# Kernel tuning notes

Hardware: AMD Instinct MI355X
Metric: run time of the kernel (lower is better)

## Reference

```python
import math
import jax, jax.numpy as jnp
import numpy as np

B, M, N, D, H = 64, 5, 1000, 128, 8
KS = D // H
TANH_CLIP = 10.0

def setup_inputs() -> dict:
    key = jax.random.key(0)
    ks = jax.random.split(key, 12)
    mask = jax.random.randint(ks[8], (B, M, N), 0, 2).astype(bool)
    mask = mask.at[:, 0, 0].set(True)  # guarantee at least one feasible action per batch row
    return {
        'node_embeddings': jax.random.normal(ks[0], (B, N, D), jnp.float32),
        'fixed_context': jax.random.normal(ks[1], (B, 1, D), jnp.float32),
        'prev_node_embeddings': jax.random.normal(ks[2], (B, M, D), jnp.float32),
        'node_dynamic_features': jax.random.normal(ks[3], (B, M, N, 8), jnp.float32),
        'vehicle_dynamic_features': jax.random.normal(ks[4], (B, M, 3), jnp.float32),
        'glimpse_V_static': jax.random.normal(ks[5], (H, B, 1, N, KS), jnp.float32),
        'glimpse_K_static': jax.random.normal(ks[6], (H, B, 1, N, KS), jnp.float32),
        'logit_K_static': jax.random.normal(ks[7], (B, 1, N, D), jnp.float32),
        'feasibility_mask': mask,
        'W_pcv': jax.random.normal(ks[9], (D, D + 3), jnp.float32) * 0.05,
        'W_pns': jax.random.normal(ks[10], (3 * D, 8), jnp.float32) * 0.05,
        'po_weight': jax.random.normal(ks[11], (D, D), jnp.float32) * 0.05,
    }

def reference(node_embeddings, fixed_context, prev_node_embeddings,
              node_dynamic_features, vehicle_dynamic_features,
              glimpse_V_static, glimpse_K_static, logit_K_static,
              feasibility_mask, W_pcv, W_pns, po_weight):
    # current vehicle state projection: [B,M,D]
    cvs = jnp.concatenate([prev_node_embeddings, vehicle_dynamic_features], axis=-1)
    proj_cvs = cvs @ W_pcv.T
    # dynamic node embeddings: [B,M,N,3D] -> three [B,M,N,D] chunks
    nde = node_dynamic_features @ W_pns.T
    gVd, gKd, lKd = jnp.split(nde, 3, axis=-1)
    # make heads: [B,M,N,D] -> [H,B,M,N,KS]
    def mh(x):
        return x.reshape(B, M, N, H, KS).transpose(3, 0, 1, 2, 4)
    glimpse_V = glimpse_V_static + mh(gVd)  # [H,B,M,N,KS]
    glimpse_K = glimpse_K_static + mh(gKd)
    logit_K = logit_K_static + lKd          # [B,M,N,D]
    query = fixed_context + proj_cvs        # [B,M,D]
    Q = query.reshape(B, M, H, KS).transpose(2, 0, 1, 3)  # [H,B,M,KS]
    mask_log = jnp.log(feasibility_mask.astype(jnp.float32))  # [B,M,N]
    compat = jnp.einsum('hbmk,hbmnk->hbmn', Q, glimpse_K) / math.sqrt(KS)
    compat = compat + mask_log[None]
    # softmax over joint vehicle*node axis
    attn = jax.nn.softmax(compat.reshape(H, B, M * N), axis=-1).reshape(H, B, M, N)
    heads = jnp.einsum('hbmn,hbmnk->hbmk', attn, glimpse_V)  # [H,B,M,KS]
    concat = heads.transpose(1, 2, 0, 3).reshape(B, M, D)
    final_Q = concat @ po_weight.T          # [B,M,D]
    logits = jnp.einsum('bmd,bmnd->bmn', final_Q, logit_K) / math.sqrt(D)
    logits = jnp.tanh(logits) * TANH_CLIP + mask_log
    probs = jax.nn.softmax(logits.reshape(B, M * N), axis=-1)
    return probs
```

## Files before the change

### kernel.cpp

```cpp
#include <hip/hip_runtime.h>
#include <cstddef>

#define BB 64
#define MM 5
#define NN 1000
#define DD 128
#define HH 8
#define KSZ 16
#define NCH 8
#define CH2 125
#define NC3 16
#define CH3 63
#define INV_SQRT_D 0.08838834764831845f

__device__ __forceinline__ float tanh_fast(float x) {
  float e = __expf(2.f * x);
  return 1.f - 2.f / (e + 1.f);
}

__global__ __launch_bounds__(256) void k1_query(
    const float* __restrict__ fc, const float* __restrict__ pne,
    const float* __restrict__ vdf, const float* __restrict__ wpcv,
    const float* __restrict__ wpns, const int* __restrict__ mask,
    float* __restrict__ q_ws, float* __restrict__ qw_ws,
    unsigned int* __restrict__ pmask)
{
  const int t = threadIdx.x;
  if (blockIdx.x >= BB * 4) {
    const int b = blockIdx.x - BB * 4;
    const int* mb = mask + (size_t)(b * MM) * NN;
    for (int n = t; n < NN; n += 256) {
      unsigned int pm = 0;
#pragma unroll
      for (int m = 0; m < MM; ++m) pm |= (mb[m * NN + n] != 0 ? 1u : 0u) << m;
      pmask[b * NN + n] = pm;
    }
    return;
  }
  const int b = blockIdx.x >> 2;
  const int dq = blockIdx.x & 3;
  const int k = t & 15, gid = t >> 4;
  __shared__ float qsh[MM][32];

  float cvr[9];
  int curm = -1;
  for (int r = 0; r < 10; ++r) {
    const int m = r >> 1;
    if (m != curm) {
      curm = m;
      const float* pner = pne + (size_t)(b * MM + m) * DD;
#pragma unroll
      for (int jp = 0; jp < 8; ++jp) cvr[jp] = pner[k + 16 * jp];
      cvr[8] = (k < 3) ? vdf[(b * MM + m) * 3 + k] : 0.f;
    }
    const int dl = (r & 1) * 16 + gid;
    const int d = dq * 32 + dl;
    const float* wrow = wpcv + d * 131;
    float p = 0.f;
#pragma unroll
    for (int jp = 0; jp < 8; ++jp) p = fmaf(cvr[jp], wrow[k + 16 * jp], p);
    if (k < 3) p = fmaf(cvr[8], wrow[128 + k], p);
    p += __shfl_xor(p, 1); p += __shfl_xor(p, 2);
    p += __shfl_xor(p, 4); p += __shfl_xor(p, 8);
    if (k == 0) {
      const float q = 0.25f * (p + fc[b * DD + d]);
      qsh[m][dl] = q;
      q_ws[(size_t)(b * MM + m) * DD + d] = q;
    }
  }
  __syncthreads();
  if (t < 80) {
    const int hh = t / 40;
    const int r = t - hh * 40, m = r >> 3, f = r & 7;
    const int h = dq * 2 + hh;
    float acc = 0.f;
#pragma unroll
    for (int kk = 0; kk < KSZ; ++kk)
      acc = fmaf(qsh[m][hh * 16 + kk], wpns[(DD + h * KSZ + kk) * 8 + f], acc);
    qw_ws[(b * HH + h) * 40 + m * 8 + f] = acc;
  }
}

__global__ __launch_bounds__(256, 4) void k2_attn(
    const float* __restrict__ ndf, const float* __restrict__ gV,
    const float* __restrict__ gK, const unsigned int* __restrict__ pmask,
    const float* __restrict__ q_ws, const float* __restrict__ qw_ws,
    float* __restrict__ part)
{
  const int blk = blockIdx.x;
  const int xcd = blk & 7;
  const int rest = blk >> 3;
  const int c = rest & 7;
  const int h = (rest >> 3) & 7;
  const int b = (rest >> 6) * 8 + xcd;
  const int t = threadIdx.x;
  const int k = t & 3, gid = t >> 2;
  const int n0 = c * CH2;

  const float* kb = gK + ((size_t)(h * BB + b) * NN + n0) * KSZ + 4 * k;
  const float* vb = gV + ((size_t)(h * BB + b) * NN + n0) * KSZ + 4 * k;
  const float* nb = ndf + ((size_t)(b * MM) * NN + n0) * 8 + 2 * k;
  const unsigned int* pmb = pmask + b * NN + n0;

  const int n1 = gid;
  const bool v2 = (gid < CH2 - 64);
  const int n2 = v2 ? gid + 64 : 0;
  const unsigned int pm1 = pmb[n1];
  const unsigned int pm2 = v2 ? pmb[n2] : 0u;
  const float4 kv1 = *(const float4*)(kb + n1 * KSZ);
  const float4 kv2 = *(const float4*)(kb + n2 * KSZ);
  const float4 vv1 = *(const float4*)(vb + n1 * KSZ);
  const float4 vv2 = *(const float4*)(vb + n2 * KSZ);
  float2 nd1[MM], nd2[MM];
#pragma unroll
  for (int m = 0; m < MM; ++m) {
    nd1[m] = *(const float2*)(nb + ((size_t)m * NN + n1) * 8);
    nd2[m] = *(const float2*)(nb + ((size_t)m * NN + n2) * 8);
  }

  float4 qr[MM];
  float2 qwr[MM];
#pragma unroll
  for (int m = 0; m < MM; ++m) {
    qr[m] = *(const float4*)(q_ws + (size_t)(b * MM + m) * DD + h * KSZ + 4 * k);
    qwr[m] = *(const float2*)(qw_ws + (b * HH + h) * 40 + m * 8 + 2 * k);
  }

  float4 hacc[MM] = {};
  float2 afv[MM] = {};
  float lsum = 0.f;

#pragma unroll
  for (int m = 0; m < MM; ++m) {
    float p = kv1.x * qr[m].x + kv1.y * qr[m].y
            + kv1.z * qr[m].z + kv1.w * qr[m].w
            + nd1[m].x * qwr[m].x + nd1[m].y * qwr[m].y;
    p += __shfl_xor(p, 1); p += __shfl_xor(p, 2);
    const float e = ((pm1 >> m) & 1u) ? __expf(p) : 0.f;
    hacc[m].x = fmaf(e, vv1.x, hacc[m].x);
    hacc[m].y = fmaf(e, vv1.y, hacc[m].y);
    hacc[m].z = fmaf(e, vv1.z, hacc[m].z);
    hacc[m].w = fmaf(e, vv1.w, hacc[m].w);
    afv[m].x = fmaf(e, nd1[m].x, afv[m].x);
    afv[m].y = fmaf(e, nd1[m].y, afv[m].y);
    lsum += e;
  }
#pragma unroll
  for (int m = 0; m < MM; ++m) {
    float p = kv2.x * qr[m].x + kv2.y * qr[m].y
            + kv2.z * qr[m].z + kv2.w * qr[m].w
            + nd2[m].x * qwr[m].x + nd2[m].y * qwr[m].y;
    p += __shfl_xor(p, 1); p += __shfl_xor(p, 2);
    const float e = ((pm2 >> m) & 1u) ? __expf(p) : 0.f;
    hacc[m].x = fmaf(e, vv2.x, hacc[m].x);
    hacc[m].y = fmaf(e, vv2.y, hacc[m].y);
    hacc[m].z = fmaf(e, vv2.z, hacc[m].z);
    hacc[m].w = fmaf(e, vv2.w, hacc[m].w);
    afv[m].x = fmaf(e, nd2[m].x, afv[m].x);
    afv[m].y = fmaf(e, nd2[m].y, afv[m].y);
    lsum += e;
  }

#pragma unroll
  for (int m = 0; m < MM; ++m) {
#pragma unroll
    for (int off = 4; off <= 32; off <<= 1) {
      hacc[m].x += __shfl_xor(hacc[m].x, off);
      hacc[m].y += __shfl_xor(hacc[m].y, off);
      hacc[m].z += __shfl_xor(hacc[m].z, off);
      hacc[m].w += __shfl_xor(hacc[m].w, off);
      afv[m].x += __shfl_xor(afv[m].x, off);
      afv[m].y += __shfl_xor(afv[m].y, off);
    }
  }
#pragma unroll
  for (int off = 4; off <= 32; off <<= 1) lsum += __shfl_xor(lsum, off);

  __shared__ float redh[4][MM][KSZ];
  __shared__ float redaf[4][MM][8];
  __shared__ float reds[4];
  const int w = t >> 6;
  if ((t & 63) < 4) {
    const int kk = t & 3;
#pragma unroll
    for (int m = 0; m < MM; ++m) {
      redh[w][m][4 * kk + 0] = hacc[m].x;
      redh[w][m][4 * kk + 1] = hacc[m].y;
      redh[w][m][4 * kk + 2] = hacc[m].z;
      redh[w][m][4 * kk + 3] = hacc[m].w;
      redaf[w][m][2 * kk + 0] = afv[m].x;
      redaf[w][m][2 * kk + 1] = afv[m].y;
    }
  }
  if ((t & 63) == 0) reds[w] = lsum;
  __syncthreads();
  float* P = part + (size_t)((b * NCH + c) * HH + h) * 128;
  if (t < 80) {
    const int m = t >> 4, kk = t & 15;
    P[t] = redh[0][m][kk] + redh[1][m][kk] + redh[2][m][kk] + redh[3][m][kk];
  } else if (t < 120) {
    const int r = t - 80, m = r >> 3, f = r & 7;
    P[80 + r] = redaf[0][m][f] + redaf[1][m][f] + redaf[2][m][f] + redaf[3][m][f];
  } else if (t == 120) {
    P[120] = reds[0] + reds[1] + reds[2] + reds[3];
  }
}

__global__ __launch_bounds__(256) void k2b_combine(
    const float* __restrict__ part, const float* __restrict__ wpns,
    const float* __restrict__ po, float* __restrict__ fq_ws,
    float* __restrict__ fw_ws)
{
  const int b = blockIdx.x;
  const int t = threadIdx.x;
  __shared__ float pos[DD][129];
  __shared__ float rgs[HH];
  __shared__ float afs[HH][MM][8];
  __shared__ float cs[MM][DD];
  __shared__ float fqs[MM][DD];

  for (int i = t; i < DD * DD / 4; i += 256) {
    const float4 v = ((const float4*)po)[i];
    const int r = (i * 4) >> 7, cc = (i * 4) & 127;
    pos[r][cc] = v.x; pos[r][cc + 1] = v.y; pos[r][cc + 2] = v.z; pos[r][cc + 3] = v.w;
  }
  const float* pb = part + (size_t)b * NCH * HH * 128;
  if (t < HH) {
    float s = 0.f;
#pragma unroll
    for (int c = 0; c < NCH; ++c) s += pb[(c * HH + t) * 128 + 120];
    rgs[t] = 1.f / s;
  }
  for (int idx = t; idx < HH * MM * 8; idx += 256) {
    const int h = idx / 40, r = idx % 40;
    float a = 0.f;
#pragma unroll
    for (int c = 0; c < NCH; ++c) a += pb[(c * HH + h) * 128 + 80 + r];
    afs[h][r >> 3][r & 7] = a;
  }
  __syncthreads();
  for (int idx = t; idx < MM * DD; idx += 256) {
    const int m = idx >> 7, d = idx & 127, h = d >> 4;
    float a = 0.f;
#pragma unroll
    for (int c = 0; c < NCH; ++c) a += pb[(c * HH + h) * 128 + m * 16 + (d & 15)];
    float cf = 0.f;
#pragma unroll
    for (int f = 0; f < 8; ++f) cf = fmaf(wpns[d * 8 + f], afs[h][m][f], cf);
    cs[m][d] = (a + cf) * rgs[h];
  }
  __syncthreads();
  for (int idx = t; idx < MM * DD; idx += 256) {
    const int m = idx >> 7, d = idx & 127;
    float acc = 0.f;
#pragma unroll 8
    for (int j = 0; j < DD; ++j) acc = fmaf(cs[m][j], pos[d][j], acc);
    acc *= INV_SQRT_D;
    fqs[m][d] = acc;
    fq_ws[(size_t)b * (MM * DD) + idx] = acc;
  }
  __syncthreads();
  if (t < MM * 8) {
    const int m = t >> 3, f = t & 7;
    float acc = 0.f;
#pragma unroll 16
    for (int d = 0; d < DD; ++d) acc = fmaf(fqs[m][d], wpns[(2 * DD + d) * 8 + f], acc);
    fw_ws[b * 40 + t] = acc;
  }
}

__global__ __launch_bounds__(256, 4) void k3_logits(
    const float* __restrict__ ndf, const float* __restrict__ lK,
    const unsigned int* __restrict__ pmask, const float* __restrict__ fq_ws,
    const float* __restrict__ fw_ws, float* __restrict__ out,
    float* __restrict__ stats)
{
  const int b = blockIdx.x & 63;
  const int c = blockIdx.x >> 6;
  const int t = threadIdx.x;
  const int k = t & 15, gid = t >> 4;
  const int n0 = c * CH3;

  float4 fqr[MM][2];
  float fwr[MM];
#pragma unroll
  for (int m = 0; m < MM; ++m) {
    fqr[m][0] = *(const float4*)(fq_ws + (size_t)(b * MM + m) * DD + 8 * k);
    fqr[m][1] = *(const float4*)(fq_ws + (size_t)(b * MM + m) * DD + 8 * k + 4);
    fwr[m] = fw_ws[b * 40 + m * 8 + (k & 7)];
  }
  float lsum = 0.f;

#pragma unroll
  for (int half = 0; half < 2; ++half) {
    float4 l0[2], l1[2];
    float ndv[2][MM];
    unsigned int pm[2];
    int ng[2];
    bool vld[2];
#pragma unroll
    for (int j = 0; j < 2; ++j) {
      const int nl = gid + 16 * (half * 2 + j);
      const int n = n0 + nl;
      vld[j] = (nl < CH3) && (n < NN);
      const int nc = vld[j] ? n : n0;
      ng[j] = nc;
      pm[j] = vld[j] ? pmask[b * NN + nc] : 0u;
      const float* lkr = lK + ((size_t)b * NN + nc) * DD;
      l0[j] = *(const float4*)(lkr + 8 * k);
      l1[j] = *(const float4*)(lkr + 8 * k + 4);
#pragma unroll
      for (int m = 0; m < MM; ++m)
        ndv[j][m] = (k < 8) ? ndf[((size_t)(b * MM + m) * NN + nc) * 8 + k] : 0.f;
    }
#pragma unroll
    for (int j = 0; j < 2; ++j) {
#pragma unroll
      for (int m = 0; m < MM; ++m) {
        float p = l0[j].x * fqr[m][0].x + l0[j].y * fqr[m][0].y
                + l0[j].z * fqr[m][0].z + l0[j].w * fqr[m][0].w
                + l1[j].x * fqr[m][1].x + l1[j].y * fqr[m][1].y
                + l1[j].z * fqr[m][1].z + l1[j].w * fqr[m][1].w
                + ndv[j][m] * fwr[m];
        p += __shfl_xor(p, 1); p += __shfl_xor(p, 2);
        p += __shfl_xor(p, 4); p += __shfl_xor(p, 8);
        const float e = ((pm[j] >> m) & 1u) ? __expf(tanh_fast(p) * 10.f) : 0.f;
        if (vld[j]) {
          lsum += e;
          if (k == 0) out[(size_t)(b * MM + m) * NN + ng[j]] = e;
        }
      }
    }
  }
  lsum += __shfl_xor(lsum, 16);
  lsum += __shfl_xor(lsum, 32);
  __shared__ float wred[4];
  if ((t & 63) == 0) wred[t >> 6] = lsum;
  __syncthreads();
  if (t == 0)
    stats[b * NC3 + c] = wred[0] + wred[1] + wred[2] + wred[3];
}

__global__ __launch_bounds__(256) void k4_probs(
    const float* __restrict__ stats, float* __restrict__ out)
{
  const int bm = blockIdx.x;
  const int b = bm / MM;
  const int t = threadIdx.x;
  float s = 0.f;
#pragma unroll
  for (int c = 0; c < NC3; ++c) s += stats[b * NC3 + c];
  const float scale = 1.f / s;
  if (t < 250) {
    float4* p = (float4*)(out + (size_t)bm * NN);
    float4 v = p[t];
    v.x *= scale; v.y *= scale; v.z *= scale; v.w *= scale;
    p[t] = v;
  }
}

extern "C" void kernel_launch(void* const* d_in, const int* in_sizes, int n_in,
                              void* d_out, int out_size, void* d_ws, size_t ws_size,
                              hipStream_t stream) {
  const float* fc   = (const float*)d_in[1];
  const float* pne  = (const float*)d_in[2];
  const float* ndf  = (const float*)d_in[3];
  const float* vdf  = (const float*)d_in[4];
  const float* gV   = (const float*)d_in[5];
  const float* gK   = (const float*)d_in[6];
  const float* lK   = (const float*)d_in[7];
  const int*   mask = (const int*)d_in[8];
  const float* wpcv = (const float*)d_in[9];
  const float* wpns = (const float*)d_in[10];
  const float* po   = (const float*)d_in[11];

  float* q_ws  = (float*)d_ws;
  float* qw_ws = q_ws + BB * MM * DD;
  float* part  = qw_ws + BB * HH * 40;
  float* fq_ws = part + (size_t)BB * NCH * HH * 128;
  float* fw_ws = fq_ws + BB * MM * DD;
  float* stats = fw_ws + BB * 40;
  unsigned int* pmask = (unsigned int*)(stats + BB * NC3);
  float* out   = (float*)d_out;

  k1_query<<<BB * 4 + BB, 256, 0, stream>>>(fc, pne, vdf, wpcv, wpns, mask,
                                            q_ws, qw_ws, pmask);
  k2_attn<<<BB * HH * NCH, 256, 0, stream>>>(ndf, gV, gK, pmask, q_ws, qw_ws, part);
  k2b_combine<<<BB, 256, 0, stream>>>(part, wpns, po, fq_ws, fw_ws);
  k3_logits<<<BB * NC3, 256, 0, stream>>>(ndf, lK, pmask, fq_ws, fw_ws, out, stats);
  k4_probs<<<BB * MM, 256, 0, stream>>>(stats, out);
}
```

Measured before the change: 69.03 us.

## Restructure attention kernel so each block covers all heads and stages node features in LDS

Measured after the change: 83.58 us. +21.1%, slower.

```diff
diff --git a/kernel.cpp b/kernel.cpp
--- a/kernel.cpp
+++ b/kernel.cpp
@@ -7,8 +7,8 @@
 #define DD 128
 #define HH 8
 #define KSZ 16
-#define NCH 8
-#define CH2 125
+#define NCH 16
+#define CH2 63
 #define NC3 16
 #define CH3 63
 #define INV_SQRT_D 0.08838834764831845f
@@ -81,128 +81,135 @@
   }
 }
 
-__global__ __launch_bounds__(256, 4) void k2_attn(
+__global__ __launch_bounds__(256, 3) void k2_attn(
     const float* __restrict__ ndf, const float* __restrict__ gV,
     const float* __restrict__ gK, const unsigned int* __restrict__ pmask,
     const float* __restrict__ q_ws, const float* __restrict__ qw_ws,
     float* __restrict__ part)
 {
-  const int blk = blockIdx.x;
-  const int xcd = blk & 7;
-  const int rest = blk >> 3;
-  const int c = rest & 7;
-  const int h = (rest >> 3) & 7;
-  const int b = (rest >> 6) * 8 + xcd;
-  const int t = threadIdx.x;
-  const int k = t & 3, gid = t >> 2;
+  const int bid = blockIdx.x;
+  const int xcd = bid & 7;
+  const int rr = bid >> 3;
+  const int c = rr & 15;
+  const int b = (rr >> 4) * 8 + xcd;
+  const int t = threadIdx.x;
+  const int w = t >> 6;
+  const int lane = t & 63;
+  const int k = t & 3;
+  const int gid = (t >> 2) & 15;
   const int n0 = c * CH2;
-
-  const float* kb = gK + ((size_t)(h * BB + b) * NN + n0) * KSZ + 4 * k;
-  const float* vb = gV + ((size_t)(h * BB + b) * NN + n0) * KSZ + 4 * k;
-  const float* nb = ndf + ((size_t)(b * MM) * NN + n0) * 8 + 2 * k;
-  const unsigned int* pmb = pmask + b * NN + n0;
-
-  const int n1 = gid;
-  const bool v2 = (gid < CH2 - 64);
-  const int n2 = v2 ? gid + 64 : 0;
-  const unsigned int pm1 = pmb[n1];
-  const unsigned int pm2 = v2 ? pmb[n2] : 0u;
-  const float4 kv1 = *(const float4*)(kb + n1 * KSZ);
-  const float4 kv2 = *(const float4*)(kb + n2 * KSZ);
-  const float4 vv1 = *(const float4*)(vb + n1 * KSZ);
-  const float4 vv2 = *(const float4*)(vb + n2 * KSZ);
-  float2 nd1[MM], nd2[MM];
+  const int nvalid = (NN - n0 < CH2) ? (NN - n0) : CH2;
+
+  __shared__ float nlds[CH2][MM][8];
+  __shared__ unsigned int pmlds[64];
+
+  for (int i = t; i < CH2 * MM * 2; i += 256) {
+    const int m = i / (CH2 * 2);
+    const int r2 = i - m * (CH2 * 2);
+    const int n = r2 >> 1, half = r2 & 1;
+    const int ns = (n < nvalid) ? n : (nvalid - 1);
+    const float4 v = *(const float4*)(ndf + ((size_t)(b * MM + m) * NN + n0 + ns) * 8 + 4 * half);
+    *(float4*)(&nlds[n][m][4 * half]) = v;
+  }
+  for (int i = t; i < 64; i += 256)
+    pmlds[i] = (i < nvalid) ? pmask[b * NN + n0 + i] : 0u;
+
+  const int h0 = 2 * w, h1 = 2 * w + 1;
+  float4 qr0[MM], qr1[MM];
+  float2 qw0[MM], qw1[MM];
 #pragma unroll
   for (int m = 0; m < MM; ++m) {
-    nd1[m] = *(const float2*)(nb + ((size_t)m * NN + n1) * 8);
-    nd2[m] = *(const float2*)(nb + ((size_t)m * NN + n2) * 8);
-  }
-
-  float4 qr[MM];
-  float2 qwr[MM];
+    qr0[m] = *(const float4*)(q_ws + (size_t)(b * MM + m) * DD + h0 * KSZ + 4 * k);
+    qr1[m] = *(const float4*)(q_ws + (size_t)(b * MM + m) * DD + h1 * KSZ + 4 * k);
+    qw0[m] = *(const float2*)(qw_ws + (b * HH + h0) * 40 + m * 8 + 2 * k);
+    qw1[m] = *(const float2*)(qw_ws + (b * HH + h1) * 40 + m * 8 + 2 * k);
+  }
+  __syncthreads();
+
+  const float* kb0 = gK + ((size_t)(h0 * BB + b) * NN + n0) * KSZ + 4 * k;
+  const float* vb0 = gV + ((size_t)(h0 * BB + b) * NN + n0) * KSZ + 4 * k;
+  const float* kb1 = gK + ((size_t)(h1 * BB + b) * NN + n0) * KSZ + 4 * k;
+  const float* vb1 = gV + ((size_t)(h1 * BB + b) * NN + n0) * KSZ + 4 * k;
+
+  float4 ha0[MM] = {}, ha1[MM] = {};
+  float2 af0[MM] = {}, af1[MM] = {};
+  float ls0 = 0.f, ls1 = 0.f;
+
+#pragma unroll
+  for (int i = 0; i < 4; ++i) {
+    const int nl = gid + 16 * i;
+    const int nc = (nl < nvalid) ? nl : (nvalid - 1);
+    const unsigned int pm = (nl < nvalid) ? pmlds[nl] : 0u;
+    const float4 K0 = *(const float4*)(kb0 + nc * KSZ);
+    const float4 V0 = *(const float4*)(vb0 + nc * KSZ);
+    const float4 K1 = *(const float4*)(kb1 + nc * KSZ);
+    const float4 V1 = *(const float4*)(vb1 + nc * KSZ);
+    float2 nd[MM];
+#pragma unroll
+    for (int m = 0; m < MM; ++m) nd[m] = *(const float2*)(&nlds[nc][m][2 * k]);
+#pragma unroll
+    for (int m = 0; m < MM; ++m) {
+      const float bit = ((pm >> m) & 1u) ? 1.f : 0.f;
+      float p0 = K0.x * qr0[m].x + K0.y * qr0[m].y + K0.z * qr0[m].z + K0.w * qr0[m].w
+               + nd[m].x * qw0[m].x + nd[m].y * qw0[m].y;
+      p0 += __shfl_xor(p0, 1); p0 += __shfl_xor(p0, 2);
+      const float e0 = bit * __expf(p0);
+      ha0[m].x = fmaf(e0, V0.x, ha0[m].x);
+      ha0[m].y = fmaf(e0, V0.y, ha0[m].y);
+      ha0[m].z = fmaf(e0, V0.z, ha0[m].z);
+      ha0[m].w = fmaf(e0, V0.w, ha0[m].w);
+      af0[m].x = fmaf(e0, nd[m].x, af0[m].x);
+      af0[m].y = fmaf(e0, nd[m].y, af0[m].y);
+      ls0 += e0;
+      float p1 = K1.x * qr1[m].x + K1.y * qr1[m].y + K1.z * qr1[m].z + K1.w * qr1[m].w
+               + nd[m].x * qw1[m].x + nd[m].y * qw1[m].y;
+      p1 += __shfl_xor(p1, 1); p1 += __shfl_xor(p1, 2);
+      const float e1 = bit * __expf(p1);
+      ha1[m].x = fmaf(e1, V1.x, ha1[m].x);
+      ha1[m].y = fmaf(e1, V1.y, ha1[m].y);
+      ha1[m].z = fmaf(e1, V1.z, ha1[m].z);
+      ha1[m].w = fmaf(e1, V1.w, ha1[m].w);
+      af1[m].x = fmaf(e1, nd[m].x, af1[m].x);
+      af1[m].y = fmaf(e1, nd[m].y, af1[m].y);
+      ls1 += e1;
+    }
+  }
+
 #pragma unroll
   for (int m = 0; m < MM; ++m) {
-    qr[m] = *(const float4*)(q_ws + (size_t)(b * MM + m) * DD + h * KSZ + 4 * k);
-    qwr[m] = *(const float2*)(qw_ws + (b * HH + h) * 40 + m * 8 + 2 * k);
-  }
-
-  float4 hacc[MM] = {};
-  float2 afv[MM] = {};
-  float lsum = 0.f;
-
-#pragma unroll
-  for (int m = 0; m < MM; ++m) {
-    float p = kv1.x * qr[m].x + kv1.y * qr[m].y
-            + kv1.z * qr[m].z + kv1.w * qr[m].w
-            + nd1[m].x * qwr[m].x + nd1[m].y * qwr[m].y;
-    p += __shfl_xor(p, 1); p += __shfl_xor(p, 2);
-    const float e = ((pm1 >> m) & 1u) ? __expf(p) : 0.f;
-    hacc[m].x = fmaf(e, vv1.x, hacc[m].x);
-    hacc[m].y = fmaf(e, vv1.y, hacc[m].y);
-    hacc[m].z = fmaf(e, vv1.z, hacc[m].z);
-    hacc[m].w = fmaf(e, vv1.w, hacc[m].w);
-    afv[m].x = fmaf(e, nd1[m].x, afv[m].x);
-    afv[m].y = fmaf(e, nd1[m].y, afv[m].y);
-    lsum += e;
-  }
-#pragma unroll
-  for (int m = 0; m < MM; ++m) {
-    float p = kv2.x * qr[m].x + kv2.y * qr[m].y
-            + kv2.z * qr[m].z + kv2.w * qr[m].w
-            + nd2[m].x * qwr[m].x + nd2[m].y * qwr[m].y;
-    p += __shfl_xor(p, 1); p += __shfl_xor(p, 2);
-    const float e = ((pm2 >> m) & 1u) ? __expf(p) : 0.f;
-    hacc[m].x = fmaf(e, vv2.x, hacc[m].x);
-    hacc[m].y = fmaf(e, vv2.y, hacc[m].y);
-    hacc[m].z = fmaf(e, vv2.z, hacc[m].z);
-    hacc[m].w = fmaf(e, vv2.w, hacc[m].w);
-    afv[m].x = fmaf(e, nd2[m].x, afv[m].x);
-    afv[m].y = fmaf(e, nd2[m].y, afv[m].y);
-    lsum += e;
-  }
-
-#pragma unroll
-  for (int m = 0; m < MM; ++m) {
 #pragma unroll
     for (int off = 4; off <= 32; off <<= 1) {
-      hacc[m].x += __shfl_xor(hacc[m].x, off);
-      hacc[m].y += __shfl_xor(hacc[m].y, off);
-      hacc[m].z += __shfl_xor(hacc[m].z, off);
-      hacc[m].w += __shfl_xor(hacc[m].w, off);
-      afv[m].x += __shfl_xor(afv[m].x, off);
-      afv[m].y += __shfl_xor(afv[m].y, off);
-    }
-  }
-#pragma unroll
-  for (int off = 4; off <= 32; off <<= 1) lsum += __shfl_xor(lsum, off);
-
-  __shared__ float redh[4][MM][KSZ];
-  __shared__ float redaf[4][MM][8];
-  __shared__ float reds[4];
-  const int w = t >> 6;
-  if ((t & 63) < 4) {
-    const int kk = t & 3;
+      ha0[m].x += __shfl_xor(ha0[m].x, off);
+      ha0[m].y += __shfl_xor(ha0[m].y, off);
+      ha0[m].z += __shfl_xor(ha0[m].z, off);
+      ha0[m].w += __shfl_xor(ha0[m].w, off);
+      af0[m].x += __shfl_xor(af0[m].x, off);
+      af0[m].y += __shfl_xor(af0[m].y, off);
+      ha1[m].x += __shfl_xor(ha1[m].x, off);
+      ha1[m].y += __shfl_xor(ha1[m].y, off);
+      ha1[m].z += __shfl_xor(ha1[m].z, off);
+      ha1[m].w += __shfl_xor(ha1[m].w, off);
+      af1[m].x += __shfl_xor(af1[m].x, off);
+      af1[m].y += __shfl_xor(af1[m].y, off);
+    }
+  }
+#pragma unroll
+  for (int off = 4; off <= 32; off <<= 1) {
+    ls0 += __shfl_xor(ls0, off);
+    ls1 += __shfl_xor(ls1, off);
+  }
+
+  if (lane < 4) {
+    float* P0 = part + (size_t)((b * NCH + c) * HH + h0) * 128;
+    float* P1 = part + (size_t)((b * NCH + c) * HH + h1) * 128;
 #pragma unroll
     for (int m = 0; m < MM; ++m) {
-      redh[w][m][4 * kk + 0] = hacc[m].x;
-      redh[w][m][4 * kk + 1] = hacc[m].y;
-      redh[w][m][4 * kk + 2] = hacc[m].z;
-      redh[w][m][4 * kk + 3] = hacc[m].w;
-      redaf[w][m][2 * kk + 0] = afv[m].x;
-      redaf[w][m][2 * kk + 1] = afv[m].y;
-    }
-  }
-  if ((t & 63) == 0) reds[w] = lsum;
-  __syncthreads();
-  float* P = part + (size_t)((b * NCH + c) * HH + h) * 128;
-  if (t < 80) {
-    const int m = t >> 4, kk = t & 15;
-    P[t] = redh[0][m][kk] + redh[1][m][kk] + redh[2][m][kk] + redh[3][m][kk];
-  } else if (t < 120) {
-    const int r = t - 80, m = r >> 3, f = r & 7;
-    P[80 + r] = redaf[0][m][f] + redaf[1][m][f] + redaf[2][m][f] + redaf[3][m][f];
-  } else if (t == 120) {
-    P[120] = reds[0] + reds[1] + reds[2] + reds[3];
+      *(float4*)(P0 + m * 16 + 4 * k) = ha0[m];
+      *(float4*)(P1 + m * 16 + 4 * k) = ha1[m];
+      *(float2*)(P0 + 80 + m * 8 + 2 * k) = af0[m];
+      *(float2*)(P1 + 80 + m * 8 + 2 * k) = af1[m];
+    }
+    if (k == 0) { P0[120] = ls0; P1[120] = ls1; }
   }
 }
 
@@ -385,7 +392,7 @@
 
   k1_query<<<BB * 4 + BB, 256, 0, stream>>>(fc, pne, vdf, wpcv, wpns, mask,
                                             q_ws, qw_ws, pmask);
-  k2_attn<<<BB * HH * NCH, 256, 0, stream>>>(ndf, gV, gK, pmask, q_ws, qw_ws, part);
+  k2_attn<<<BB * NCH, 256, 0, stream>>>(ndf, gV, gK, pmask, q_ws, qw_ws, part);
   k2b_combine<<<BB, 256, 0, stream>>>(part, wpns, po, fq_ws, fw_ws);
   k3_logits<<<BB * NC3, 256, 0, stream>>>(ndf, lK, pmask, fq_ws, fw_ws, out, stats);
   k4_probs<<<BB * MM, 256, 0, stream>>>(stats, out);
```
